# Kernel optimization log

Hardware: AMD Instinct MI355X
Metric: run time of the kernel (lower is better)

The kernel has to match this reference:

```python
import jax, jax.numpy as jnp
import numpy as np

BETA = 10.0  # fixed buffer: torch.ones(1, num_centers) * 10


def setup_inputs() -> dict:
    key = jax.random.key(0)
    k1, k2, k3 = jax.random.split(key, 3)
    n, M, d, n_out = 65536, 1024, 64, 3
    x = jax.random.normal(k1, (n, d), dtype=jnp.float32)
    centers = jax.random.normal(k2, (M, d), dtype=jnp.float32)
    # nn.Linear init in the module: weight ~ N(0, 0.02), bias = 0
    W = jax.random.normal(k3, (n_out, M + d), dtype=jnp.float32) * 0.02
    b = jnp.zeros((n_out,), dtype=jnp.float32)
    return {"x": x, "centers": centers, "W": W, "b": b}


def reference(x, centers, W, b):
    x2 = jnp.sum(x * x, axis=1, keepdims=True)          # [n, 1]
    c2 = jnp.sum(centers * centers, axis=1)             # [M]
    d2 = x2 + c2[None, :] - 2.0 * (x @ centers.T)       # [n, M]
    rbf = jnp.exp(-BETA * d2)                           # Gaussian RBF
    feat = jnp.concatenate([x, rbf], axis=1)            # [n, d + M]
    return feat @ W.T + b                               # [n, n_out]
```

## Files before the change

### kernel.cpp

```cpp
#include <hip/hip_runtime.h>
#include <math.h>

typedef short bf16x8 __attribute__((ext_vector_type(8)));
typedef float f32x4 __attribute__((ext_vector_type(4)));
typedef unsigned int uint32;

#define BETA 10.0f
#define THRESH -88.0f

#define C_OFF   0
#define XB_OFF  65536
#define RED_OFF 73728
#define LDS_TOT 75264

__device__ __forceinline__ uint32 f2bf_rtne(float f) {
    uint32 u = __float_as_uint(f);
    u += 0x7FFFu + ((u >> 16) & 1u);
    return u >> 16;
}
__device__ __forceinline__ uint32 pk_rtne(float a, float b) {
    return f2bf_rtne(a) | (f2bf_rtne(b) << 16);
}
__device__ __forceinline__ f32x4 vmax4(f32x4 a, f32x4 b) {
    f32x4 r;
    r[0] = fmaxf(a[0], b[0]); r[1] = fmaxf(a[1], b[1]);
    r[2] = fmaxf(a[2], b[2]); r[3] = fmaxf(a[3], b[3]);
    return r;
}
#define MFMA __builtin_amdgcn_mfma_f32_16x16x32_bf16

__global__ __launch_bounds__(512, 4) void rbfn_fused(
    const float* __restrict__ x,
    const float* __restrict__ centers,
    const float* __restrict__ W,
    const float* __restrict__ bias,
    float* __restrict__ out)
{
    __shared__ __align__(16) char lds[LDS_TOT];

    const int tid = threadIdx.x;
    const int wv = tid >> 6;
    const int lane = tid & 63;
    const int quad = lane >> 4;
    const int l15 = lane & 15;
    const int row0 = blockIdx.x * 128;
    const f32x4 z = {0.f, 0.f, 0.f, 0.f};

    #pragma unroll
    for (int i = 0; i < 16; ++i) {
        const int f = i * 512 + tid;
        const int j = f >> 3, sg = f & 7;
        const float4 v = *((const float4*)centers + j * 16 + sg);
        uint2 q;
        q.x = pk_rtne(20.f * v.x, 20.f * v.y);
        q.y = pk_rtne(20.f * v.z, 20.f * v.w);
        *(uint2*)(lds + C_OFF + (j >> 4) * 1024 + (sg >> 1) * 256 +
                  (j & 15) * 16 + (sg & 1) * 8) = q;
    }
    #pragma unroll
    for (int i = 0; i < 2; ++i) {
        const int f = i * 512 + tid;
        const int r = f >> 3, sg = f & 7;
        const float4 v = *((const float4*)(x + (size_t)row0 * 64) + r * 16 + sg);
        uint2 q; q.x = pk_rtne(v.x, v.y); q.y = pk_rtne(v.z, v.w);
        *(uint2*)(lds + XB_OFF + (r >> 4) * 1024 + (sg >> 1) * 256 +
                  (r & 15) * 16 + (sg & 1) * 8) = q;
    }

    {
        const int r = tid >> 2, e = tid & 3;
        const float4* xr = (const float4*)(x + (size_t)(row0 + r) * 64) + e * 4;
        const float4 a0 = xr[0], a1 = xr[1], a2 = xr[2], a3 = xr[3];
        const float4 av[4] = {a0, a1, a2, a3};
        float d0 = 0.f, d1 = 0.f, d2 = 0.f;
        #pragma unroll
        for (int i = 0; i < 4; ++i) {
            const float4 a = av[i];
            const float4 w0 = *((const float4*)(W + 0 * 1088) + e * 4 + i);
            const float4 w1 = *((const float4*)(W + 1 * 1088) + e * 4 + i);
            const float4 w2 = *((const float4*)(W + 2 * 1088) + e * 4 + i);
            d0 = fmaf(a.w, w0.w, fmaf(a.z, w0.z, fmaf(a.y, w0.y, fmaf(a.x, w0.x, d0))));
            d1 = fmaf(a.w, w1.w, fmaf(a.z, w1.z, fmaf(a.y, w1.y, fmaf(a.x, w1.x, d1))));
            d2 = fmaf(a.w, w2.w, fmaf(a.z, w2.z, fmaf(a.y, w2.y, fmaf(a.x, w2.x, d2))));
        }
        #pragma unroll
        for (int m = 1; m <= 2; m <<= 1) {
            d0 += __shfl_xor(d0, m);
            d1 += __shfl_xor(d1, m);
            d2 += __shfl_xor(d2, m);
        }
        if (e == 0) {
            float* red = (float*)(lds + RED_OFF);
            red[r * 3 + 0] = d0 + bias[0];
            red[r * 3 + 1] = d1 + bias[1];
            red[r * 3 + 2] = d2 + bias[2];
        }
    }
    __syncthreads();

    bf16x8 af[8];
    #pragma unroll
    for (int rt = 0; rt < 8; ++rt)
        af[rt] = *(const bf16x8*)(lds + XB_OFF + rt * 1024 + quad * 256 + l15 * 16);

    f32x4 pr[8];
    #pragma unroll
    for (int rt = 0; rt < 8; ++rt) {
        const f32x4 d = MFMA(af[rt], af[rt], z, 0, 0, 0);
        f32x4 p;
        #pragma unroll
        for (int reg = 0; reg < 4; ++reg)
            p[reg] = -BETA * __shfl(d[reg], quad * 20 + reg);
        pr[rt] = p;
    }

    bf16x8 bf[8];
    float c2r[8];
    #pragma unroll
    for (int ct = 0; ct < 8; ++ct) {
        bf[ct] = *(const bf16x8*)(lds + C_OFF + (wv * 8 + ct) * 1024 +
                                  quad * 256 + l15 * 16);
        const f32x4 d = MFMA(bf[ct], bf[ct], z, 0, 0, 0);
        const float dv = (l15 & 2) ? ((l15 & 1) ? d[3] : d[2])
                                   : ((l15 & 1) ? d[1] : d[0]);
        c2r[ct] = (-BETA / 400.f) * __shfl(dv, (l15 >> 2) * 16 + l15);
    }

    #pragma unroll
    for (int ct = 0; ct < 8; ++ct) {
        const bf16x8 b = bf[ct];
        f32x4 mx = {-1e30f, -1e30f, -1e30f, -1e30f};
        #pragma unroll
        for (int rt = 0; rt < 8; ++rt)
            mx = vmax4(mx, MFMA(af[rt], b, pr[rt], 0, 0, 0));
        const float bct = fmaxf(fmaxf(mx[0], mx[1]), fmaxf(mx[2], mx[3])) + c2r[ct];

        if (__builtin_expect(__ballot(bct > THRESH) != 0ull, 0)) {
            float* red = (float*)(lds + RED_OFF);
            const int j = wv * 128 + ct * 16 + l15;
            const float w0 = W[0 * 1088 + 64 + j];
            const float w1 = W[1 * 1088 + 64 + j];
            const float w2 = W[2 * 1088 + 64 + j];
            const float* cr = centers + (size_t)j * 64;
            #pragma clang loop unroll(disable)
            for (int rr = 0; rr < 32; ++rr) {
                const int r = quad * 32 + rr;
                const float* xr = x + (size_t)(row0 + r) * 64;
                float d2 = 0.f;
                #pragma clang loop unroll(disable)
                for (int k = 0; k < 64; ++k) {
                    const float df = xr[k] - cr[k];
                    d2 = fmaf(df, df, d2);
                }
                const float arg = -BETA * d2;
                if (arg > -87.f) {
                    const float e = expf(arg);
                    atomicAdd(&red[r * 3 + 0], e * w0);
                    atomicAdd(&red[r * 3 + 1], e * w1);
                    atomicAdd(&red[r * 3 + 2], e * w2);
                }
            }
        }
    }
    __syncthreads();

    if (tid < 96)
        ((float4*)out)[blockIdx.x * 96 + tid] = *((const float4*)(lds + RED_OFF) + tid);
}

extern "C" void kernel_launch(void* const* d_in, const int* in_sizes, int n_in,
                              void* d_out, int out_size, void* d_ws, size_t ws_size,
                              hipStream_t stream) {
    const float* x       = (const float*)d_in[0];
    const float* centers = (const float*)d_in[1];
    const float* W       = (const float*)d_in[2];
    const float* b       = (const float*)d_in[3];
    float* out = (float*)d_out;

    const int n = in_sizes[0] / 64;
    rbfn_fused<<<n / 128, 512, 0, stream>>>(x, centers, W, b, out);
}
```

Before: 76.30 us.

## Process two 128-row tiles per block to amortize centers staging

Each block now handles 256 rows as two 128-row tiles, reusing the bf16-converted centers in LDS and the per-wave center fragments and norms for both tiles. This halves the grid and halves the redundant conversion and loading of the 1024x64 centers matrix per row processed. In exchange, LDS per block grows, the launch bound occupancy hint drops from 4 to 2, and there are fewer blocks to spread across CUs (256 blocks), which may reduce latency hiding.

```diff
diff --git a/kernel.cpp b/kernel.cpp
--- a/kernel.cpp
+++ b/kernel.cpp
@@ -8,10 +8,12 @@
 #define BETA 10.0f
 #define THRESH -88.0f
 
-#define C_OFF   0
-#define XB_OFF  65536
-#define RED_OFF 73728
-#define LDS_TOT 75264
+#define C_OFF    0
+#define XB0_OFF  65536
+#define XB1_OFF  73728
+#define RED0_OFF 81920
+#define RED1_OFF 83456
+#define LDS_TOT  84992
 
 __device__ __forceinline__ uint32 f2bf_rtne(float f) {
     uint32 u = __float_as_uint(f);
@@ -29,7 +31,7 @@
 }
 #define MFMA __builtin_amdgcn_mfma_f32_16x16x32_bf16
 
-__global__ __launch_bounds__(512, 4) void rbfn_fused(
+__global__ __launch_bounds__(512, 2) void rbfn_fused(
     const float* __restrict__ x,
     const float* __restrict__ centers,
     const float* __restrict__ W,
@@ -43,7 +45,7 @@
     const int lane = tid & 63;
     const int quad = lane >> 4;
     const int l15 = lane & 15;
-    const int row0 = blockIdx.x * 128;
+    const int row0 = blockIdx.x * 256;
     const f32x4 z = {0.f, 0.f, 0.f, 0.f};
 
     #pragma unroll
@@ -58,18 +60,23 @@
                   (j & 15) * 16 + (sg & 1) * 8) = q;
     }
     #pragma unroll
-    for (int i = 0; i < 2; ++i) {
-        const int f = i * 512 + tid;
-        const int r = f >> 3, sg = f & 7;
-        const float4 v = *((const float4*)(x + (size_t)row0 * 64) + r * 16 + sg);
-        uint2 q; q.x = pk_rtne(v.x, v.y); q.y = pk_rtne(v.z, v.w);
-        *(uint2*)(lds + XB_OFF + (r >> 4) * 1024 + (sg >> 1) * 256 +
-                  (r & 15) * 16 + (sg & 1) * 8) = q;
+    for (int t = 0; t < 2; ++t) {
+        const int xb = t ? XB1_OFF : XB0_OFF;
+        #pragma unroll
+        for (int i = 0; i < 2; ++i) {
+            const int f = i * 512 + tid;
+            const int r = f >> 3, sg = f & 7;
+            const float4 v = *((const float4*)(x + (size_t)(row0 + t * 128) * 64) + r * 16 + sg);
+            uint2 q; q.x = pk_rtne(v.x, v.y); q.y = pk_rtne(v.z, v.w);
+            *(uint2*)(lds + xb + (r >> 4) * 1024 + (sg >> 1) * 256 +
+                      (r & 15) * 16 + (sg & 1) * 8) = q;
+        }
     }
 
-    {
+    #pragma unroll
+    for (int t = 0; t < 2; ++t) {
         const int r = tid >> 2, e = tid & 3;
-        const float4* xr = (const float4*)(x + (size_t)(row0 + r) * 64) + e * 4;
+        const float4* xr = (const float4*)(x + (size_t)(row0 + t * 128 + r) * 64) + e * 4;
         const float4 a0 = xr[0], a1 = xr[1], a2 = xr[2], a3 = xr[3];
         const float4 av[4] = {a0, a1, a2, a3};
         float d0 = 0.f, d1 = 0.f, d2 = 0.f;
@@ -90,29 +97,13 @@
             d2 += __shfl_xor(d2, m);
         }
         if (e == 0) {
-            float* red = (float*)(lds + RED_OFF);
+            float* red = (float*)(lds + (t ? RED1_OFF : RED0_OFF));
             red[r * 3 + 0] = d0 + bias[0];
             red[r * 3 + 1] = d1 + bias[1];
             red[r * 3 + 2] = d2 + bias[2];
         }
     }
     __syncthreads();
-
-    bf16x8 af[8];
-    #pragma unroll
-    for (int rt = 0; rt < 8; ++rt)
-        af[rt] = *(const bf16x8*)(lds + XB_OFF + rt * 1024 + quad * 256 + l15 * 16);
-
-    f32x4 pr[8];
-    #pragma unroll
-    for (int rt = 0; rt < 8; ++rt) {
-        const f32x4 d = MFMA(af[rt], af[rt], z, 0, 0, 0);
-        f32x4 p;
-        #pragma unroll
-        for (int reg = 0; reg < 4; ++reg)
-            p[reg] = -BETA * __shfl(d[reg], quad * 20 + reg);
-        pr[rt] = p;
-    }
 
     bf16x8 bf[8];
     float c2r[8];
@@ -127,45 +118,70 @@
     }
 
     #pragma unroll
-    for (int ct = 0; ct < 8; ++ct) {
-        const bf16x8 b = bf[ct];
-        f32x4 mx = {-1e30f, -1e30f, -1e30f, -1e30f};
+    for (int t = 0; t < 2; ++t) {
+        const int xb = t ? XB1_OFF : XB0_OFF;
+        float* red = (float*)(lds + (t ? RED1_OFF : RED0_OFF));
+
+        bf16x8 af[8];
         #pragma unroll
         for (int rt = 0; rt < 8; ++rt)
-            mx = vmax4(mx, MFMA(af[rt], b, pr[rt], 0, 0, 0));
-        const float bct = fmaxf(fmaxf(mx[0], mx[1]), fmaxf(mx[2], mx[3])) + c2r[ct];
+            af[rt] = *(const bf16x8*)(lds + xb + rt * 1024 + quad * 256 + l15 * 16);
 
-        if (__builtin_expect(__ballot(bct > THRESH) != 0ull, 0)) {
-            float* red = (float*)(lds + RED_OFF);
-            const int j = wv * 128 + ct * 16 + l15;
-            const float w0 = W[0 * 1088 + 64 + j];
-            const float w1 = W[1 * 1088 + 64 + j];
-            const float w2 = W[2 * 1088 + 64 + j];
-            const float* cr = centers + (size_t)j * 64;
-            #pragma clang loop unroll(disable)
-            for (int rr = 0; rr < 32; ++rr) {
-                const int r = quad * 32 + rr;
-                const float* xr = x + (size_t)(row0 + r) * 64;
-                float d2 = 0.f;
+        f32x4 pr[8];
+        #pragma unroll
+        for (int rt = 0; rt < 8; ++rt) {
+            const f32x4 d = MFMA(af[rt], af[rt], z, 0, 0, 0);
+            f32x4 p;
+            #pragma unroll
+            for (int reg = 0; reg < 4; ++reg)
+                p[reg] = -BETA * __shfl(d[reg], quad * 20 + reg);
+            pr[rt] = p;
+        }
+
+        #pragma unroll
+        for (int ct = 0; ct < 8; ++ct) {
+            const bf16x8 b = bf[ct];
+            f32x4 mx = {-1e30f, -1e30f, -1e30f, -1e30f};
+            #pragma unroll
+            for (int rt = 0; rt < 8; ++rt)
+                mx = vmax4(mx, MFMA(af[rt], b, pr[rt], 0, 0, 0));
+            const float bct = fmaxf(fmaxf(mx[0], mx[1]), fmaxf(mx[2], mx[3])) + c2r[ct];
+
+            if (__builtin_expect(__ballot(bct > THRESH) != 0ull, 0)) {
+                const int j = wv * 128 + ct * 16 + l15;
+                const float w0 = W[0 * 1088 + 64 + j];
+                const float w1 = W[1 * 1088 + 64 + j];
+                const float w2 = W[2 * 1088 + 64 + j];
+                const float* cr = centers + (size_t)j * 64;
                 #pragma clang loop unroll(disable)
-                for (int k = 0; k < 64; ++k) {
-                    const float df = xr[k] - cr[k];
-                    d2 = fmaf(df, df, d2);
-                }
-                const float arg = -BETA * d2;
-                if (arg > -87.f) {
-                    const float e = expf(arg);
-                    atomicAdd(&red[r * 3 + 0], e * w0);
-                    atomicAdd(&red[r * 3 + 1], e * w1);
-                    atomicAdd(&red[r * 3 + 2], e * w2);
+                for (int rr = 0; rr < 32; ++rr) {
+                    const int r = quad * 32 + rr;
+                    const float* xr = x + (size_t)(row0 + t * 128 + r) * 64;
+                    float d2 = 0.f;
+                    #pragma clang loop unroll(disable)
+                    for (int k = 0; k < 64; ++k) {
+                        const float df = xr[k] - cr[k];
+                        d2 = fmaf(df, df, d2);
+                    }
+                    const float arg = -BETA * d2;
+                    if (arg > -87.f) {
+                        const float e = expf(arg);
+                        atomicAdd(&red[r * 3 + 0], e * w0);
+                        atomicAdd(&red[r * 3 + 1], e * w1);
+                        atomicAdd(&red[r * 3 + 2], e * w2);
+                    }
                 }
             }
         }
     }
     __syncthreads();
 
-    if (tid < 96)
-        ((float4*)out)[blockIdx.x * 96 + tid] = *((const float4*)(lds + RED_OFF) + tid);
+    if (tid < 96) {
+        ((float4*)out)[blockIdx.x * 192 + tid] =
+            *((const float4*)(lds + RED0_OFF) + tid);
+        ((float4*)out)[blockIdx.x * 192 + 96 + tid] =
+            *((const float4*)(lds + RED1_OFF) + tid);
+    }
 }
 
 extern "C" void kernel_launch(void* const* d_in, const int* in_sizes, int n_in,
@@ -178,5 +194,5 @@
     float* out = (float*)d_out;
 
     const int n = in_sizes[0] / 64;
-    rbfn_fused<<<n / 128, 512, 0, stream>>>(x, centers, W, b, out);
+    rbfn_fused<<<n / 256, 512, 0, stream>>>(x, centers, W, b, out);
 }
```

New measurement: 75.31 us. No clear change (-1.3%).
